# Kernel tuning notes

Measured on AMD Instinct MI355X. Metric: run time of the kernel, lower is better.

Reference implementation:

```python
import jax, jax.numpy as jnp
import numpy as np

DIM = 512
HEADS = 8
DIM_HEAD = 32
INNER = HEADS * DIM_HEAD  # 256
B, N = 2, 2048
EPS = 1e-5


def setup_inputs() -> dict:
    key = jax.random.key(0)
    ks = jax.random.split(key, 6)
    x = jax.random.normal(ks[0], (B, N, DIM), dtype=jnp.float32)
    rel_pos_bias = jax.random.normal(ks[1], (HEADS, N, N), dtype=jnp.float32)
    ln_scale = jnp.ones((DIM,), dtype=jnp.float32)
    w_qkv = jax.random.normal(ks[2], (DIM, INNER * 3), dtype=jnp.float32) / np.sqrt(DIM)
    w_out = jax.random.normal(ks[3], (INNER, DIM), dtype=jnp.float32) / np.sqrt(INNER)
    b_out = jnp.zeros((DIM,), dtype=jnp.float32)
    return {"x": x, "rel_pos_bias": rel_pos_bias, "ln_scale": ln_scale,
            "w_qkv": w_qkv, "w_out": w_out, "b_out": b_out}


def reference(x, rel_pos_bias, ln_scale, w_qkv, w_out, b_out):
    scale = DIM_HEAD ** -0.5
    # LayerNorm (no bias), eps=1e-5
    mu = jnp.mean(x, axis=-1, keepdims=True)
    var = jnp.mean(jnp.square(x - mu), axis=-1, keepdims=True)
    xn = (x - mu) * jax.lax.rsqrt(var + EPS) * ln_scale
    # fused QKV projection, no bias
    qkv = xn @ w_qkv  # [b, n, 3*inner]
    q, k, v = jnp.split(qkv, 3, axis=-1)
    def to_heads(t):
        b, n, _ = t.shape
        return t.reshape(b, n, HEADS, DIM_HEAD).transpose(0, 2, 1, 3)  # b h n d
    q, k, v = map(to_heads, (q, k, v))
    q = q * scale
    sim = jnp.einsum('bhid,bhjd->bhij', q, k)
    sim = sim + rel_pos_bias  # (h,n,n) broadcasts over batch
    attn = jax.nn.softmax(sim, axis=-1)
    o = jnp.einsum('bhij,bhjd->bhid', attn, v)
    o = o.transpose(0, 2, 1, 3).reshape(x.shape[0], x.shape[1], INNER)  # b n (h d)
    return o @ w_out + b_out
```

## Files before the change

### kernel.cpp

```cpp
#include <hip/hip_runtime.h>
#include <hip/hip_bf16.h>
#include <cstdint>

#define NB 2
#define NSEQ 2048
#define NDIM 512
#define NHEAD 8
#define DHEAD 32
#define NINNER 256
#define NQKV 768
#define LNEPS 1e-5f
#define QSCALE 0.17677669529663687f

typedef short short8 __attribute__((ext_vector_type(8)));
typedef float f32x4 __attribute__((ext_vector_type(4)));
typedef unsigned int u32x4 __attribute__((ext_vector_type(4)));
typedef unsigned int u32x2 __attribute__((ext_vector_type(2)));
typedef unsigned short u16;
typedef unsigned int u32;

__device__ __forceinline__ f32x4 mfma16(short8 a, short8 b, f32x4 c) {
    return __builtin_amdgcn_mfma_f32_16x16x32_bf16(a, b, c, 0, 0, 0);
}

__device__ __forceinline__ u16 f2bf(float a) {
    union { float f; u32 u; } x; x.f = a;
    u32 r = x.u + 0x7fffu + ((x.u >> 16) & 1u);
    return (u16)(r >> 16);
}
__device__ __forceinline__ float bf2f(u16 h) {
    union { float f; u32 u; } x; x.u = ((u32)h) << 16; return x.f;
}
__device__ __forceinline__ void split2(float a, u16& hi, u16& lo) {
    hi = f2bf(a);
    lo = f2bf(a - bf2f(hi));
}
__device__ __forceinline__ u32 pk2(float a, float b) {
    return (u32)f2bf(a) | ((u32)f2bf(b) << 16);
}

__global__ __launch_bounds__(256) void ln_kernel(
    const float* __restrict__ x, const float* __restrict__ gamma,
    u32* __restrict__ xn_hi, u32* __restrict__ xn_lo)
{
    const int row = blockIdx.x;
    const int t = threadIdx.x;
    const float2 v = ((const float2*)(x + (size_t)row * NDIM))[t];
    float s1 = v.x + v.y;
    float s2 = v.x * v.x + v.y * v.y;
    #pragma unroll
    for (int off = 32; off >= 1; off >>= 1) {
        s1 += __shfl_down(s1, off);
        s2 += __shfl_down(s2, off);
    }
    __shared__ float a1[4], a2[4];
    if ((t & 63) == 0) { a1[t >> 6] = s1; a2[t >> 6] = s2; }
    __syncthreads();
    const float ts1 = a1[0] + a1[1] + a1[2] + a1[3];
    const float ts2 = a2[0] + a2[1] + a2[2] + a2[3];
    const float mu = ts1 * (1.0f / NDIM);
    const float var = ts2 * (1.0f / NDIM) - mu * mu;
    const float rs = rsqrtf(var + LNEPS);
    const float2 g = ((const float2*)gamma)[t];
    u16 h0, l0, h1, l1;
    split2((v.x - mu) * rs * g.x, h0, l0);
    split2((v.y - mu) * rs * g.y, h1, l1);
    xn_hi[(size_t)row * (NDIM / 2) + t] = (u32)h0 | ((u32)h1 << 16);
    xn_lo[(size_t)row * (NDIM / 2) + t] = (u32)l0 | ((u32)l1 << 16);
}

__global__ __launch_bounds__(256) void wtrans_kernel(
    const float* __restrict__ wq, u16* __restrict__ wqT_hi, u16* __restrict__ wqT_lo,
    const float* __restrict__ wo, u16* __restrict__ woT_hi, u16* __restrict__ woT_lo)
{
    __shared__ __align__(16) u16 th[64][72], tl[64][72];
    const int t = threadIdx.x;
    const float* w; u16 *wT_hi, *wT_lo; int K, N, k0, n0;
    if (blockIdx.x < 96) {
        w = wq; wT_hi = wqT_hi; wT_lo = wqT_lo; K = NDIM; N = NQKV;
        k0 = (blockIdx.x & 7) * 64; n0 = (blockIdx.x >> 3) * 64;
    } else {
        const int b = blockIdx.x - 96;
        w = wo; wT_hi = woT_hi; wT_lo = woT_lo; K = NINNER; N = NDIM;
        k0 = (b & 3) * 64; n0 = (b >> 2) * 64;
    }
    {
        const int k = t >> 2, c = (t & 3) * 16;
        const float* src = w + (size_t)(k0 + k) * N + n0 + c;
        #pragma unroll
        for (int jj = 0; jj < 4; jj++) {
            const f32x4 w4 = *(const f32x4*)(src + jj * 4);
            #pragma unroll
            for (int e = 0; e < 4; e++) {
                u16 hh, ll;
                split2(w4[e], hh, ll);
                th[k][c + jj * 4 + e] = hh;
                tl[k][c + jj * 4 + e] = ll;
            }
        }
    }
    __syncthreads();
    {
        const int n = t >> 2, kc = (t & 3) * 16;
        u16 hb[16], lb[16];
        #pragma unroll
        for (int j = 0; j < 16; j++) { hb[j] = th[kc + j][n]; lb[j] = tl[kc + j][n]; }
        u16* dh = wT_hi + (size_t)(n0 + n) * K + k0 + kc;
        u16* dl = wT_lo + (size_t)(n0 + n) * K + k0 + kc;
        *(short8*)dh = *(short8*)hb;
        *(short8*)(dh + 8) = *(short8*)(hb + 8);
        *(short8*)dl = *(short8*)lb;
        *(short8*)(dl + 8) = *(short8*)(lb + 8);
    }
}

__global__ __launch_bounds__(256) void vtrans_kernel(
    const u16* __restrict__ v, u16* __restrict__ vt)
{
    __shared__ __align__(16) u16 sh[64][40];
    const int t = threadIdx.x;
    const int n0 = blockIdx.x * 64;
    const int bh = blockIdx.y;
    {
        const int n = t >> 2, c = (t & 3) * 8;
        *(short8*)&sh[n][c] = *(const short8*)(v + ((size_t)bh * NSEQ + n0 + n) * DHEAD + c);
    }
    __syncthreads();
    {
        const int d = t >> 3, nc = (t & 7) * 8;
        u16 buf[8];
        #pragma unroll
        for (int j = 0; j < 8; j++) buf[j] = sh[nc + j][d];
        *(short8*)(vt + ((size_t)bh * DHEAD + d) * NSEQ + n0 + nc) = *(short8*)buf;
    }
}

__global__ __launch_bounds__(256, 4) void qkv_kernel(
    const u16* __restrict__ xn_hi, const u16* __restrict__ xn_lo,
    const u16* __restrict__ wT_hi, const u16* __restrict__ wT_lo,
    u16* __restrict__ q_hi, u16* __restrict__ q_lo,
    u16* __restrict__ k_hi, u16* __restrict__ k_lo,
    u16* __restrict__ v)
{
    __shared__ __align__(16) u16 Ah[64][40], Al[64][40], Bh[64][40], Bl[64][40];
    const int t = threadIdx.x;
    const int wave = t >> 6, lane = t & 63;
    const int lrow = lane & 15, lquad = lane >> 4;
    const int rowBase = blockIdx.x * 64;
    const int colBase = blockIdx.y * 64;
    const int wm = (wave & 1) * 32;
    const int wn = (wave >> 1) * 32;
    const int kf = lquad * 8;
    const f32x4 zero = {0.f, 0.f, 0.f, 0.f};
    f32x4 acc[2][2];
    acc[0][0] = zero; acc[0][1] = zero; acc[1][0] = zero; acc[1][1] = zero;

    const int sr = t >> 2, sc = (t & 3) * 8;

    for (int k0 = 0; k0 < NDIM; k0 += 32) {
        __syncthreads();
        *(short8*)&Ah[sr][sc] = *(const short8*)(xn_hi + (size_t)(rowBase + sr) * NDIM + k0 + sc);
        *(short8*)&Al[sr][sc] = *(const short8*)(xn_lo + (size_t)(rowBase + sr) * NDIM + k0 + sc);
        *(short8*)&Bh[sr][sc] = *(const short8*)(wT_hi + (size_t)(colBase + sr) * NDIM + k0 + sc);
        *(short8*)&Bl[sr][sc] = *(const short8*)(wT_lo + (size_t)(colBase + sr) * NDIM + k0 + sc);
        __syncthreads();
        const short8 a0h = *(const short8*)&Ah[wm + lrow][kf];
        const short8 a0l = *(const short8*)&Al[wm + lrow][kf];
        const short8 a1h = *(const short8*)&Ah[wm + 16 + lrow][kf];
        const short8 a1l = *(const short8*)&Al[wm + 16 + lrow][kf];
        const short8 b0h = *(const short8*)&Bh[wn + lrow][kf];
        const short8 b0l = *(const short8*)&Bl[wn + lrow][kf];
        const short8 b1h = *(const short8*)&Bh[wn + 16 + lrow][kf];
        const short8 b1l = *(const short8*)&Bl[wn + 16 + lrow][kf];
        acc[0][0] = mfma16(a0h, b0h, acc[0][0]); acc[0][0] = mfma16(a0h, b0l, acc[0][0]); acc[0][0] = mfma16(a0l, b0h, acc[0][0]);
        acc[0][1] = mfma16(a0h, b1h, acc[0][1]); acc[0][1] = mfma16(a0h, b1l, acc[0][1]); acc[0][1] = mfma16(a0l, b1h, acc[0][1]);
        acc[1][0] = mfma16(a1h, b0h, acc[1][0]); acc[1][0] = mfma16(a1h, b0l, acc[1][0]); acc[1][0] = mfma16(a1l, b0h, acc[1][0]);
        acc[1][1] = mfma16(a1h, b1h, acc[1][1]); acc[1][1] = mfma16(a1h, b1l, acc[1][1]); acc[1][1] = mfma16(a1l, b1h, acc[1][1]);
    }

    #pragma unroll
    for (int mi = 0; mi < 2; mi++) {
        #pragma unroll
        for (int ni = 0; ni < 2; ni++) {
            #pragma unroll
            for (int r = 0; r < 4; r++) {
                const int grow = rowBase + wm + mi * 16 + lquad * 4 + r;
                const int gcol = colBase + wn + ni * 16 + lrow;
                const float val = acc[mi][ni][r];
                const int bidx = grow >> 11;
                const int n = grow & (NSEQ - 1);
                const int sec = gcol >> 8;
                const int idx = gcol & 255;
                const int head = idx >> 5, d = idx & 31;
                const int bh = bidx * NHEAD + head;
                if (sec == 0) {
                    u16 hh, ll;
                    split2(val * QSCALE, hh, ll);
                    const size_t a = ((size_t)bh * NSEQ + n) * DHEAD + d;
                    q_hi[a] = hh; q_lo[a] = ll;
                } else if (sec == 1) {
                    u16 hh, ll;
                    split2(val, hh, ll);
                    const size_t a = ((size_t)bh * NSEQ + n) * DHEAD + d;
                    k_hi[a] = hh; k_lo[a] = ll;
                } else {
                    v[((size_t)bh * NSEQ + n) * DHEAD + d] = f2bf(val);
                }
            }
        }
    }
}

__global__ __launch_bounds__(512, 4) void attn_kernel(
    const u16* __restrict__ q_hi, const u16* __restrict__ q_lo,
    const u16* __restrict__ k_hi, const u16* __restrict__ k_lo,
    const u16* __restrict__ vt,
    const float* __restrict__ bias,
    u16* __restrict__ o_hi, u16* __restrict__ o_lo)
{
    __shared__ __align__(16) float cA[2][8][64][4];
    __shared__ __align__(16) float cB[2][8][64][4];
    __shared__ float cl[2][8][16];
    const int t = threadIdx.x;
    const int wave = t >> 6, lane = t & 63;
    const int lrow = lane & 15, lquad = lane >> 4;
    const int kslice = wave;
    const int bh = blockIdx.y;
    const int batch = bh >> 3, head = bh & 7;
    const int qb = blockIdx.x * 32;
    const size_t qkb = (size_t)bh * NSEQ * DHEAD;
    const size_t qoff0 = (size_t)(qb + lrow) * DHEAD + lquad * 8;
    const size_t qoff1 = (size_t)(qb + 16 + lrow) * DHEAD + lquad * 8;
    const short8 qh0 = *(const short8*)(q_hi + qkb + qoff0);
    const short8 ql0 = *(const short8*)(q_lo + qkb + qoff0);
    const short8 qh1 = *(const short8*)(q_hi + qkb + qoff1);
    const short8 ql1 = *(const short8*)(q_lo + qkb + qoff1);
    const f32x4 zero = {0.f, 0.f, 0.f, 0.f};
    f32x4 accA0 = zero, accB0 = zero, accA1 = zero, accB1 = zero;
    float lp0 = 0.f, lp1 = 0.f;
    const int kperm = ((lrow >> 2) << 3) | (lrow & 3);
    const float* bptr0 = bias + (size_t)head * NSEQ * NSEQ + (size_t)(qb + lrow) * NSEQ;
    const float* bptr1 = bptr0 + 16 * NSEQ;
    const int kt0 = kslice * 256;

    f32x4 b00 = *(const f32x4*)(bptr0 + kt0 + lquad * 8);
    f32x4 b01 = *(const f32x4*)(bptr0 + kt0 + lquad * 8 + 4);
    f32x4 b10 = *(const f32x4*)(bptr1 + kt0 + lquad * 8);
    f32x4 b11 = *(const f32x4*)(bptr1 + kt0 + lquad * 8 + 4);

    for (int i = 0; i < 8; i++) {
        const int kt = kt0 + i * 32;
        const size_t kof = (size_t)(kt + kperm) * DHEAD + lquad * 8;
        const short8 k0h = *(const short8*)(k_hi + qkb + kof);
        const short8 k0l = *(const short8*)(k_lo + qkb + kof);
        const short8 k1h = *(const short8*)(k_hi + qkb + kof + 4 * DHEAD);
        const short8 k1l = *(const short8*)(k_lo + qkb + kof + 4 * DHEAD);
        const short8 va0 = *(const short8*)(vt + qkb + (size_t)lrow * NSEQ + kt + lquad * 8);
        const short8 va1 = *(const short8*)(vt + qkb + (size_t)(16 + lrow) * NSEQ + kt + lquad * 8);
        const int ktn = kt0 + ((i + 1) & 7) * 32;
        const f32x4 nb00 = *(const f32x4*)(bptr0 + ktn + lquad * 8);
        const f32x4 nb01 = *(const f32x4*)(bptr0 + ktn + lquad * 8 + 4);
        const f32x4 nb10 = *(const f32x4*)(bptr1 + ktn + lquad * 8);
        const f32x4 nb11 = *(const f32x4*)(bptr1 + ktn + lquad * 8 + 4);

        {
            f32x4 c0 = zero, c1 = zero;
            c0 = mfma16(k0h, qh0, c0); c0 = mfma16(k0h, ql0, c0); c0 = mfma16(k0l, qh0, c0);
            c1 = mfma16(k1h, qh0, c1); c1 = mfma16(k1h, ql0, c1); c1 = mfma16(k1l, qh0, c1);
            f32x4 p0, p1;
            #pragma unroll
            for (int r = 0; r < 4; r++) {
                p0[r] = __expf(c0[r] + b00[r]);
                p1[r] = __expf(c1[r] + b01[r]);
            }
            lp0 += (p0[0] + p0[1]) + (p0[2] + p0[3]) + (p1[0] + p1[1]) + (p1[2] + p1[3]);
            union { u32x4 u; short8 s; } cv;
            cv.u[0] = pk2(p0[0], p0[1]);
            cv.u[1] = pk2(p0[2], p0[3]);
            cv.u[2] = pk2(p1[0], p1[1]);
            cv.u[3] = pk2(p1[2], p1[3]);
            accA0 = mfma16(va0, cv.s, accA0);
            accB0 = mfma16(va1, cv.s, accB0);
        }
        {
            f32x4 c0 = zero, c1 = zero;
            c0 = mfma16(k0h, qh1, c0); c0 = mfma16(k0h, ql1, c0); c0 = mfma16(k0l, qh1, c0);
            c1 = mfma16(k1h, qh1, c1); c1 = mfma16(k1h, ql1, c1); c1 = mfma16(k1l, qh1, c1);
            f32x4 p0, p1;
            #pragma unroll
            for (int r = 0; r < 4; r++) {
                p0[r] = __expf(c0[r] + b10[r]);
                p1[r] = __expf(c1[r] + b11[r]);
            }
            lp1 += (p0[0] + p0[1]) + (p0[2] + p0[3]) + (p1[0] + p1[1]) + (p1[2] + p1[3]);
            union { u32x4 u; short8 s; } cv;
            cv.u[0] = pk2(p0[0], p0[1]);
            cv.u[1] = pk2(p0[2], p0[3]);
            cv.u[2] = pk2(p1[0], p1[1]);
            cv.u[3] = pk2(p1[2], p1[3]);
            accA1 = mfma16(va0, cv.s, accA1);
            accB1 = mfma16(va1, cv.s, accB1);
        }
        b00 = nb00; b01 = nb01; b10 = nb10; b11 = nb11;
    }

    lp0 += __shfl_xor(lp0, 16); lp0 += __shfl_xor(lp0, 32);
    lp1 += __shfl_xor(lp1, 16); lp1 += __shfl_xor(lp1, 32);

    *(f32x4*)&cA[0][kslice][lane][0] = accA0;
    *(f32x4*)&cB[0][kslice][lane][0] = accB0;
    *(f32x4*)&cA[1][kslice][lane][0] = accA1;
    *(f32x4*)&cB[1][kslice][lane][0] = accB1;
    if (lquad == 0) {
        cl[0][kslice][lrow] = lp0;
        cl[1][kslice][lrow] = lp1;
    }
    __syncthreads();
    if (wave < 4) {
        const int s = wave >> 1, part = wave & 1;
        const float (*src)[64][4] = part ? (const float (*)[64][4])cB[s]
                                         : (const float (*)[64][4])cA[s];
        f32x4 sv = *(const f32x4*)&src[0][lane][0];
        #pragma unroll
        for (int w = 1; w < 8; w++) {
            sv += *(const f32x4*)&src[w][lane][0];
        }
        float lt = 0.f;
        #pragma unroll
        for (int w = 0; w < 8; w++) lt += cl[s][w][lrow];
        const float inv = 1.0f / lt;
        const int q = qb + s * 16 + lrow;
        const size_t base = ((size_t)batch * NSEQ + q) * NINNER + head * DHEAD + part * 16 + lquad * 4;
        u16 h[4], l[4];
        #pragma unroll
        for (int r = 0; r < 4; r++) {
            split2(sv[r] * inv, h[r], l[r]);
        }
        *(u32x2*)&o_hi[base] = *(u32x2*)&h[0];
        *(u32x2*)&o_lo[base] = *(u32x2*)&l[0];
    }
}

__global__ __launch_bounds__(256, 4) void out_kernel(
    const u16* __restrict__ o_hi, const u16* __restrict__ o_lo,
    const u16* __restrict__ wT_hi, const u16* __restrict__ wT_lo,
    const float* __restrict__ b_out,
    float* __restrict__ out)
{
    __shared__ __align__(16) u16 Ah[64][40], Al[64][40], Bh[64][40], Bl[64][40];
    const int t = threadIdx.x;
    const int wave = t >> 6, lane = t & 63;
    const int lrow = lane & 15, lquad = lane >> 4;
    const int rowBase = blockIdx.x * 64;
    const int colBase = blockIdx.y * 64;
    const int wm = (wave & 1) * 32;
    const int wn = (wave >> 1) * 32;
    const int kf = lquad * 8;
    const f32x4 zero = {0.f, 0.f, 0.f, 0.f};
    f32x4 acc[2][2];
    acc[0][0] = zero; acc[0][1] = zero; acc[1][0] = zero; acc[1][1] = zero;

    const int sr = t >> 2, sc = (t & 3) * 8;

    for (int k0 = 0; k0 < NINNER; k0 += 32) {
        __syncthreads();
        *(short8*)&Ah[sr][sc] = *(const short8*)(o_hi + (size_t)(rowBase + sr) * NINNER + k0 + sc);
        *(short8*)&Al[sr][sc] = *(const short8*)(o_lo + (size_t)(rowBase + sr) * NINNER + k0 + sc);
        *(short8*)&Bh[sr][sc] = *(const short8*)(wT_hi + (size_t)(colBase + sr) * NINNER + k0 + sc);
        *(short8*)&Bl[sr][sc] = *(const short8*)(wT_lo + (size_t)(colBase + sr) * NINNER + k0 + sc);
        __syncthreads();
        const short8 a0h = *(const short8*)&Ah[wm + lrow][kf];
        const short8 a0l = *(const short8*)&Al[wm + lrow][kf];
        const short8 a1h = *(const short8*)&Ah[wm + 16 + lrow][kf];
        const short8 a1l = *(const short8*)&Al[wm + 16 + lrow][kf];
        const short8 b0h = *(const short8*)&Bh[wn + lrow][kf];
        const short8 b0l = *(const short8*)&Bl[wn + lrow][kf];
        const short8 b1h = *(const short8*)&Bh[wn + 16 + lrow][kf];
        const short8 b1l = *(const short8*)&Bl[wn + 16 + lrow][kf];
        acc[0][0] = mfma16(a0h, b0h, acc[0][0]); acc[0][0] = mfma16(a0h, b0l, acc[0][0]); acc[0][0] = mfma16(a0l, b0h, acc[0][0]);
        acc[0][1] = mfma16(a0h, b1h, acc[0][1]); acc[0][1] = mfma16(a0h, b1l, acc[0][1]); acc[0][1] = mfma16(a0l, b1h, acc[0][1]);
        acc[1][0] = mfma16(a1h, b0h, acc[1][0]); acc[1][0] = mfma16(a1h, b0l, acc[1][0]); acc[1][0] = mfma16(a1l, b0h, acc[1][0]);
        acc[1][1] = mfma16(a1h, b1h, acc[1][1]); acc[1][1] = mfma16(a1h, b1l, acc[1][1]); acc[1][1] = mfma16(a1l, b1h, acc[1][1]);
    }

    #pragma unroll
    for (int mi = 0; mi < 2; mi++) {
        #pragma unroll
        for (int ni = 0; ni < 2; ni++) {
            #pragma unroll
            for (int r = 0; r < 4; r++) {
                const int grow = rowBase + wm + mi * 16 + lquad * 4 + r;
                const int gcol = colBase + wn + ni * 16 + lrow;
                out[(size_t)grow * NDIM + gcol] = acc[mi][ni][r] + b_out[gcol];
            }
        }
    }
}

extern "C" void kernel_launch(void* const* d_in, const int* in_sizes, int n_in,
                              void* d_out, int out_size, void* d_ws, size_t ws_size,
                              hipStream_t stream)
{
    (void)in_sizes; (void)n_in; (void)out_size; (void)ws_size;
    const float* x     = (const float*)d_in[0];
    const float* bias  = (const float*)d_in[1];
    const float* gamma = (const float*)d_in[2];
    const float* wqkv  = (const float*)d_in[3];
    const float* wout  = (const float*)d_in[4];
    const float* bout  = (const float*)d_in[5];
    float* out = (float*)d_out;

    char* ws = (char*)d_ws;
    size_t off = 0;
    auto carve = [&](size_t bytes) -> void* {
        void* p = (void*)(ws + off);
        off += (bytes + 255) & ~(size_t)255;
        return p;
    };
    const size_t rows = (size_t)NB * NSEQ;
    const size_t hn = (size_t)NB * NHEAD * NSEQ * DHEAD;
    u16* xn_hi = (u16*)carve(rows * NDIM * 2);
    u16* xn_lo = (u16*)carve(rows * NDIM * 2);
    u16* wqT_hi = (u16*)carve((size_t)NQKV * NDIM * 2);
    u16* wqT_lo = (u16*)carve((size_t)NQKV * NDIM * 2);
    u16* woT_hi = (u16*)carve((size_t)NDIM * NINNER * 2);
    u16* woT_lo = (u16*)carve((size_t)NDIM * NINNER * 2);
    u16* q_hi  = (u16*)carve(hn * 2);
    u16* q_lo  = (u16*)carve(hn * 2);
    u16* k_hi  = (u16*)carve(hn * 2);
    u16* k_lo  = (u16*)carve(hn * 2);
    u16* vbuf  = (u16*)carve(hn * 2);
    u16* vt    = (u16*)carve(hn * 2);
    u16* o_hi  = (u16*)carve(rows * NINNER * 2);
    u16* o_lo  = (u16*)carve(rows * NINNER * 2);

    ln_kernel<<<dim3((unsigned)rows), 256, 0, stream>>>(x, gamma, (u32*)xn_hi, (u32*)xn_lo);
    wtrans_kernel<<<dim3(128), 256, 0, stream>>>(wqkv, wqT_hi, wqT_lo, wout, woT_hi, woT_lo);
    qkv_kernel<<<dim3(64, 12), 256, 0, stream>>>(xn_hi, xn_lo, wqT_hi, wqT_lo,
                                                 q_hi, q_lo, k_hi, k_lo, vbuf);
    vtrans_kernel<<<dim3(NSEQ / 64, NB * NHEAD), 256, 0, stream>>>(vbuf, vt);
    attn_kernel<<<dim3(NSEQ / 32, NB * NHEAD), 512, 0, stream>>>(q_hi, q_lo, k_hi, k_lo,
                                                                 vt, bias, o_hi, o_lo);
    out_kernel<<<dim3(64, 8), 256, 0, stream>>>(o_hi, o_lo, woT_hi, woT_lo, bout, out);
}
```

Measured before the change: 280.3 us.

## Process both batches per attention block to share rel_pos_bias loads

The attention kernel now assigns the two batch elements to alternating waves inside one block, so the grid covers only heads, not batch times heads. Each wave handles a 512-key slice instead of 256, and the cross-wave reduction now sums four slices per batch. The aim is for the two batch waves reading the same bias rows to hit in cache, cutting global traffic for the large fp32 bias tensor roughly in half. In exchange the grid has half as many blocks and each wave runs a longer serial loop, which lowers parallelism.

```diff
diff --git a/kernel.cpp b/kernel.cpp
--- a/kernel.cpp
+++ b/kernel.cpp
@@ -218,17 +218,16 @@
     const float* __restrict__ bias,
     u16* __restrict__ o_hi, u16* __restrict__ o_lo)
 {
-    __shared__ __align__(16) float cA[2][8][64][4];
-    __shared__ __align__(16) float cB[2][8][64][4];
-    __shared__ float cl[2][8][16];
+    __shared__ __align__(16) float cA[2][2][4][64][4];
+    __shared__ __align__(16) float cB[2][2][4][64][4];
+    __shared__ float cl[2][2][4][16];
     const int t = threadIdx.x;
     const int wave = t >> 6, lane = t & 63;
     const int lrow = lane & 15, lquad = lane >> 4;
-    const int kslice = wave;
-    const int bh = blockIdx.y;
-    const int batch = bh >> 3, head = bh & 7;
+    const int batch = wave & 1, kslice = wave >> 1;
+    const int head = blockIdx.y;
     const int qb = blockIdx.x * 32;
-    const size_t qkb = (size_t)bh * NSEQ * DHEAD;
+    const size_t qkb = (size_t)(batch * NHEAD + head) * NSEQ * DHEAD;
     const size_t qoff0 = (size_t)(qb + lrow) * DHEAD + lquad * 8;
     const size_t qoff1 = (size_t)(qb + 16 + lrow) * DHEAD + lquad * 8;
     const short8 qh0 = *(const short8*)(q_hi + qkb + qoff0);
@@ -241,14 +240,14 @@
     const int kperm = ((lrow >> 2) << 3) | (lrow & 3);
     const float* bptr0 = bias + (size_t)head * NSEQ * NSEQ + (size_t)(qb + lrow) * NSEQ;
     const float* bptr1 = bptr0 + 16 * NSEQ;
-    const int kt0 = kslice * 256;
+    const int kt0 = kslice * 512;
 
     f32x4 b00 = *(const f32x4*)(bptr0 + kt0 + lquad * 8);
     f32x4 b01 = *(const f32x4*)(bptr0 + kt0 + lquad * 8 + 4);
     f32x4 b10 = *(const f32x4*)(bptr1 + kt0 + lquad * 8);
     f32x4 b11 = *(const f32x4*)(bptr1 + kt0 + lquad * 8 + 4);
 
-    for (int i = 0; i < 8; i++) {
+    for (int i = 0; i < 16; i++) {
         const int kt = kt0 + i * 32;
         const size_t kof = (size_t)(kt + kperm) * DHEAD + lquad * 8;
         const short8 k0h = *(const short8*)(k_hi + qkb + kof);
@@ -257,7 +256,7 @@
         const short8 k1l = *(const short8*)(k_lo + qkb + kof + 4 * DHEAD);
         const short8 va0 = *(const short8*)(vt + qkb + (size_t)lrow * NSEQ + kt + lquad * 8);
         const short8 va1 = *(const short8*)(vt + qkb + (size_t)(16 + lrow) * NSEQ + kt + lquad * 8);
-        const int ktn = kt0 + ((i + 1) & 7) * 32;
+        const int ktn = kt0 + ((i + 1) & 15) * 32;
         const f32x4 nb00 = *(const f32x4*)(bptr0 + ktn + lquad * 8);
         const f32x4 nb01 = *(const f32x4*)(bptr0 + ktn + lquad * 8 + 4);
         const f32x4 nb10 = *(const f32x4*)(bptr1 + ktn + lquad * 8);
@@ -307,30 +306,29 @@
     lp0 += __shfl_xor(lp0, 16); lp0 += __shfl_xor(lp0, 32);
     lp1 += __shfl_xor(lp1, 16); lp1 += __shfl_xor(lp1, 32);
 
-    *(f32x4*)&cA[0][kslice][lane][0] = accA0;
-    *(f32x4*)&cB[0][kslice][lane][0] = accB0;
-    *(f32x4*)&cA[1][kslice][lane][0] = accA1;
-    *(f32x4*)&cB[1][kslice][lane][0] = accB1;
+    *(f32x4*)&cA[batch][0][kslice][lane][0] = accA0;
+    *(f32x4*)&cB[batch][0][kslice][lane][0] = accB0;
+    *(f32x4*)&cA[batch][1][kslice][lane][0] = accA1;
+    *(f32x4*)&cB[batch][1][kslice][lane][0] = accB1;
     if (lquad == 0) {
-        cl[0][kslice][lrow] = lp0;
-        cl[1][kslice][lrow] = lp1;
+        cl[batch][0][kslice][lrow] = lp0;
+        cl[batch][1][kslice][lrow] = lp1;
     }
     __syncthreads();
-    if (wave < 4) {
-        const int s = wave >> 1, part = wave & 1;
-        const float (*src)[64][4] = part ? (const float (*)[64][4])cB[s]
-                                         : (const float (*)[64][4])cA[s];
+    {
+        const int bb = wave & 1, s = (wave >> 1) & 1, part = wave >> 2;
+        const float (*src)[64][4] = part ? (const float (*)[64][4])cB[bb][s]
+                                         : (const float (*)[64][4])cA[bb][s];
         f32x4 sv = *(const f32x4*)&src[0][lane][0];
         #pragma unroll
-        for (int w = 1; w < 8; w++) {
+        for (int w = 1; w < 4; w++) {
             sv += *(const f32x4*)&src[w][lane][0];
         }
-        float lt = 0.f;
-        #pragma unroll
-        for (int w = 0; w < 8; w++) lt += cl[s][w][lrow];
+        const float lt = cl[bb][s][0][lrow] + cl[bb][s][1][lrow]
+                       + cl[bb][s][2][lrow] + cl[bb][s][3][lrow];
         const float inv = 1.0f / lt;
         const int q = qb + s * 16 + lrow;
-        const size_t base = ((size_t)batch * NSEQ + q) * NINNER + head * DHEAD + part * 16 + lquad * 4;
+        const size_t base = ((size_t)bb * NSEQ + q) * NINNER + head * DHEAD + part * 16 + lquad * 4;
         u16 h[4], l[4];
         #pragma unroll
         for (int r = 0; r < 4; r++) {
@@ -439,7 +437,7 @@
     qkv_kernel<<<dim3(64, 12), 256, 0, stream>>>(xn_hi, xn_lo, wqT_hi, wqT_lo,
                                                  q_hi, q_lo, k_hi, k_lo, vbuf);
     vtrans_kernel<<<dim3(NSEQ / 64, NB * NHEAD), 256, 0, stream>>>(vbuf, vt);
-    attn_kernel<<<dim3(NSEQ / 32, NB * NHEAD), 512, 0, stream>>>(q_hi, q_lo, k_hi, k_lo,
-                                                                 vt, bias, o_hi, o_lo);
+    attn_kernel<<<dim3(NSEQ / 32, NHEAD), 512, 0, stream>>>(q_hi, q_lo, k_hi, k_lo,
+                                                            vt, bias, o_hi, o_lo);
     out_kernel<<<dim3(64, 8), 256, 0, stream>>>(o_hi, o_lo, woT_hi, woT_lo, bout, out);
 }
```

Result: no change. 274.9 us, median of 2 (-1.9%).
